# Performance work log

Measured on AMD Instinct MI355X. Metric: run time of the kernel, lower is better.

Reference implementation:

```python
import jax, jax.numpy as jnp
import numpy as np

GROUPS = 8


def setup_inputs() -> dict:
    key = jax.random.key(0)
    k1, k2, k3 = jax.random.split(key, 3)
    B, H, W, Cin, Cout, KH, KW = 32, 56, 56, 256, 256, 3, 3
    inputs = jax.random.normal(k1, (B, H, W, Cin), dtype=jnp.float32)
    # HWIO kernel for grouped conv: input channel dim = Cin // groups
    fan_in = KH * KW * (Cin // GROUPS)
    limit = np.sqrt(6.0 / (fan_in + Cout // GROUPS))  # glorot-ish scale
    kernel = jax.random.uniform(k2, (KH, KW, Cin // GROUPS, Cout), dtype=jnp.float32,
                                minval=-limit, maxval=limit)
    bias = jnp.zeros((Cout,), dtype=jnp.float32)
    return {"inputs": inputs, "kernel": kernel, "bias": bias}


def reference(inputs, kernel, bias):
    # Equivalent to per-group slice + Conv2D + concat: a single grouped conv.
    # inputs: [B,H,W,Cin] NHWC; kernel: [KH,KW,Cin//G,Cout] HWIO
    out = jax.lax.conv_general_dilated(
        inputs, kernel,
        window_strides=(1, 1),
        padding="SAME",
        lhs_dilation=(1, 1),
        rhs_dilation=(1, 1),
        dimension_numbers=("NHWC", "HWIO", "NHWC"),
        feature_group_count=GROUPS,
    )
    out = out + bias  # broadcast over [B,H,W,Cout]
    return out
```

## Files before the change

kernel.cpp:

```cpp
#include <hip/hip_runtime.h>


#define R_ 8
#define TPW 7

typedef __bf16 bf16x8 __attribute__((ext_vector_type(8)));
typedef float floatx4 __attribute__((ext_vector_type(4)));
typedef unsigned short ushortx4 __attribute__((ext_vector_type(4)));

__device__ __forceinline__ unsigned short f2bf(float f) {
    unsigned int u = __builtin_bit_cast(unsigned int, f);
    u += 0x7fffu + ((u >> 16) & 1u);
    return (unsigned short)(u >> 16);
}

__global__ __launch_bounds__(256)
void wprep(const float* __restrict__ wgt, unsigned short* __restrict__ wbf) {
    const int i = blockIdx.x * 256 + threadIdx.x;
    const int co256 = i & 255;
    const int tmp   = i >> 8;
    const int ci    = tmp & 31;
    const int kk    = tmp >> 5;
    const int g  = co256 >> 5;
    const int co = co256 & 31;
    wbf[((g * 9 + kk) * 32 + co) * 32 + ci] = f2bf(wgt[i]);
}

__global__ __launch_bounds__(256, 4)
void gconv_mfma(const float* __restrict__ in, const unsigned short* __restrict__ wbf,
                const float* __restrict__ bias, float* __restrict__ out) {
    const int rt = blockIdx.x;
    const int g  = blockIdx.y;
    const int b  = blockIdx.z;
    const int y0 = rt * R_;

    __shared__ unsigned short lds_in[10 * 58 * 32];

    const int tid = threadIdx.x;

    for (int c = tid; c < 10 * 58 * 8; c += 256) {
        const int row = c / 464;
        const int rem = c - row * 464;
        const int col = rem >> 3;
        const int q   = rem & 7;
        const int gy = y0 - 1 + row;
        const int gx = col - 1;
        float4 v = make_float4(0.f, 0.f, 0.f, 0.f);
        if ((unsigned)gy < 56u && (unsigned)gx < 56u) {
            v = *reinterpret_cast<const float4*>(
                &in[(((b * 56 + gy) * 56 + gx) * 256) + g * 32 + q * 4]);
        }
        ushortx4 p;
        p.x = f2bf(v.x); p.y = f2bf(v.y); p.z = f2bf(v.z); p.w = f2bf(v.w);
        *reinterpret_cast<ushortx4*>(&lds_in[(row * 58 + col) * 32 + q * 4]) = p;
    }

    __syncthreads();

    const int wv   = tid >> 6;
    const int lane = tid & 63;
    const int lc   = lane & 15;
    const int quad = lane >> 4;

    int lane_base[TPW];
#pragma unroll
    for (int t = 0; t < TPW; ++t) {
        const int p  = (wv * TPW + t) * 16 + lc;
        const int yl = p / 56;
        const int xl = p - yl * 56;
        lane_base[t] = (yl * 58 + xl) * 32 + quad * 8;
    }

    const unsigned short* wq = &wbf[((g * 9) * 32) * 32 + quad * 8];

    floatx4 acc[TPW][2];
#pragma unroll
    for (int t = 0; t < TPW; ++t) {
        acc[t][0] = (floatx4)(0.f);
        acc[t][1] = (floatx4)(0.f);
    }

    bf16x8 b0 = *reinterpret_cast<const bf16x8*>(&wq[(0 * 32 + lc) * 32]);
    bf16x8 b1 = *reinterpret_cast<const bf16x8*>(&wq[(0 * 32 + 16 + lc) * 32]);

#pragma unroll
    for (int kk = 0; kk < 9; ++kk) {
        const int ky = kk / 3, kx = kk % 3;
        const int koff = (ky * 58 + kx) * 32;
        bf16x8 nb0 = b0, nb1 = b1;
        if (kk < 8) {
            nb0 = *reinterpret_cast<const bf16x8*>(&wq[((kk + 1) * 32 + lc) * 32]);
            nb1 = *reinterpret_cast<const bf16x8*>(&wq[((kk + 1) * 32 + 16 + lc) * 32]);
        }
#pragma unroll
        for (int t = 0; t < TPW; ++t) {
            const bf16x8 a = *reinterpret_cast<const bf16x8*>(&lds_in[lane_base[t] + koff]);
            acc[t][0] = __builtin_amdgcn_mfma_f32_16x16x32_bf16(a, b0, acc[t][0], 0, 0, 0);
            acc[t][1] = __builtin_amdgcn_mfma_f32_16x16x32_bf16(a, b1, acc[t][1], 0, 0, 0);
        }
        b0 = nb0; b1 = nb1;
    }

    const float bv0 = bias[g * 32 + lc];
    const float bv1 = bias[g * 32 + 16 + lc];
#pragma unroll
    for (int t = 0; t < TPW; ++t) {
#pragma unroll
        for (int r = 0; r < 4; ++r) {
            const int p = (wv * TPW + t) * 16 + quad * 4 + r;
            const int y = p / 56;
            const int x = p - y * 56;
            float* o = &out[(((b * 56) + y0 + y) * 56 + x) * 256 + g * 32];
            o[lc]      = acc[t][0][r] + bv0;
            o[16 + lc] = acc[t][1][r] + bv1;
        }
    }
}

__global__ __launch_bounds__(256, 2)
void gconv_mfma_ldsw(const float* __restrict__ in, const float* __restrict__ wgt,
                     const float* __restrict__ bias, float* __restrict__ out) {
    const int rt = blockIdx.x, g = blockIdx.y, b = blockIdx.z;
    const int y0 = rt * R_;
    __shared__ unsigned short lds_in[10 * 58 * 32];
    __shared__ unsigned short lds_w[9 * 32 * 32];
    const int tid = threadIdx.x;
    for (int i = tid; i < 9 * 32 * 32; i += 256) {
        const int co = i & 31, ci = (i >> 5) & 31, kk = i >> 10;
        lds_w[(kk * 32 + co) * 32 + ci] = f2bf(wgt[(kk * 32 + ci) * 256 + g * 32 + co]);
    }
    for (int c = tid; c < 10 * 58 * 8; c += 256) {
        const int row = c / 464, rem = c - row * 464, col = rem >> 3, q = rem & 7;
        const int gy = y0 - 1 + row, gx = col - 1;
        float4 v = make_float4(0.f, 0.f, 0.f, 0.f);
        if ((unsigned)gy < 56u && (unsigned)gx < 56u)
            v = *reinterpret_cast<const float4*>(&in[(((b * 56 + gy) * 56 + gx) * 256) + g * 32 + q * 4]);
        ushortx4 p;
        p.x = f2bf(v.x); p.y = f2bf(v.y); p.z = f2bf(v.z); p.w = f2bf(v.w);
        *reinterpret_cast<ushortx4*>(&lds_in[(row * 58 + col) * 32 + q * 4]) = p;
    }
    __syncthreads();
    const int wv = tid >> 6, lane = tid & 63, lc = lane & 15, quad = lane >> 4;
    int lane_base[TPW];
#pragma unroll
    for (int t = 0; t < TPW; ++t) {
        const int p = (wv * TPW + t) * 16 + lc;
        const int yl = p / 56, xl = p - yl * 56;
        lane_base[t] = (yl * 58 + xl) * 32 + quad * 8;
    }
    floatx4 acc[TPW][2];
#pragma unroll
    for (int t = 0; t < TPW; ++t) { acc[t][0] = (floatx4)(0.f); acc[t][1] = (floatx4)(0.f); }
#pragma unroll
    for (int kk = 0; kk < 9; ++kk) {
        const int ky = kk / 3, kx = kk % 3;
        const int koff = (ky * 58 + kx) * 32;
        const bf16x8 bf0 = *reinterpret_cast<const bf16x8*>(&lds_w[(kk * 32 + lc) * 32 + quad * 8]);
        const bf16x8 bf1 = *reinterpret_cast<const bf16x8*>(&lds_w[(kk * 32 + 16 + lc) * 32 + quad * 8]);
#pragma unroll
        for (int t = 0; t < TPW; ++t) {
            const bf16x8 a = *reinterpret_cast<const bf16x8*>(&lds_in[lane_base[t] + koff]);
            acc[t][0] = __builtin_amdgcn_mfma_f32_16x16x32_bf16(a, bf0, acc[t][0], 0, 0, 0);
            acc[t][1] = __builtin_amdgcn_mfma_f32_16x16x32_bf16(a, bf1, acc[t][1], 0, 0, 0);
        }
    }
    const float bv0 = bias[g * 32 + lc], bv1 = bias[g * 32 + 16 + lc];
#pragma unroll
    for (int t = 0; t < TPW; ++t)
#pragma unroll
        for (int r = 0; r < 4; ++r) {
            const int p = (wv * TPW + t) * 16 + quad * 4 + r;
            const int y = p / 56, x = p - y * 56;
            float* o = &out[(((b * 56) + y0 + y) * 56 + x) * 256 + g * 32];
            o[lc] = acc[t][0][r] + bv0;
            o[16 + lc] = acc[t][1][r] + bv1;
        }
}

extern "C" void kernel_launch(void* const* d_in, const int* in_sizes, int n_in,
                              void* d_out, int out_size, void* d_ws, size_t ws_size,
                              hipStream_t stream) {
    const float* in   = (const float*)d_in[0];
    const float* wgt  = (const float*)d_in[1];
    const float* bias = (const float*)d_in[2];
    float* out        = (float*)d_out;
    dim3 grid(7, 8, 32);

    if (ws_size >= (size_t)(8 * 9 * 32 * 32 * sizeof(unsigned short))) {
        unsigned short* wbf = (unsigned short*)d_ws;
        wprep<<<dim3(288, 1, 1), dim3(256, 1, 1), 0, stream>>>(wgt, wbf);
        gconv_mfma<<<grid, dim3(256, 1, 1), 0, stream>>>(in, wbf, bias, out);
    } else {
        gconv_mfma_ldsw<<<grid, dim3(256, 1, 1), 0, stream>>>(in, wgt, bias, out);
    }
}
```

Before: 198.1 us.

## Halve row tile, raise occupancy, swap MFMA operands for vectorized float4 stores

The main MFMA kernel now processes 4 output rows per block instead of 8, giving twice as many blocks and a smaller LDS tile. The launch bound is raised to 7 blocks per CU. The 14 pixel tiles are split unevenly across waves (4,4,3,3). MFMA operands are swapped so each lane holds 4 consecutive output channels, which lets the epilogue write float4 stores and read bias as float4 instead of issuing scalar scattered writes. The cost is more halo reloading per output row and idle waves on the shorter tile counts.

```diff
diff --git a/kernel.cpp b/kernel.cpp
--- a/kernel.cpp
+++ b/kernel.cpp
@@ -1,8 +1,8 @@
 #include <hip/hip_runtime.h>
 
 
-#define R_ 8
-#define TPW 7
+#define R_ 4
+#define NCHUNK (6 * 58 * 8)
 
 typedef __bf16 bf16x8 __attribute__((ext_vector_type(8)));
 typedef float floatx4 __attribute__((ext_vector_type(4)));
@@ -26,7 +26,7 @@
     wbf[((g * 9 + kk) * 32 + co) * 32 + ci] = f2bf(wgt[i]);
 }
 
-__global__ __launch_bounds__(256, 4)
+__global__ __launch_bounds__(256, 7)
 void gconv_mfma(const float* __restrict__ in, const unsigned short* __restrict__ wbf,
                 const float* __restrict__ bias, float* __restrict__ out) {
     const int rt = blockIdx.x;
@@ -34,25 +34,29 @@
     const int b  = blockIdx.z;
     const int y0 = rt * R_;
 
-    __shared__ unsigned short lds_in[10 * 58 * 32];
+    __shared__ unsigned short lds_in[6 * 58 * 32];
 
     const int tid = threadIdx.x;
 
-    for (int c = tid; c < 10 * 58 * 8; c += 256) {
-        const int row = c / 464;
-        const int rem = c - row * 464;
-        const int col = rem >> 3;
-        const int q   = rem & 7;
-        const int gy = y0 - 1 + row;
-        const int gx = col - 1;
-        float4 v = make_float4(0.f, 0.f, 0.f, 0.f);
-        if ((unsigned)gy < 56u && (unsigned)gx < 56u) {
-            v = *reinterpret_cast<const float4*>(
-                &in[(((b * 56 + gy) * 56 + gx) * 256) + g * 32 + q * 4]);
-        }
-        ushortx4 p;
-        p.x = f2bf(v.x); p.y = f2bf(v.y); p.z = f2bf(v.z); p.w = f2bf(v.w);
-        *reinterpret_cast<ushortx4*>(&lds_in[(row * 58 + col) * 32 + q * 4]) = p;
+#pragma unroll
+    for (int i = 0; i < 11; ++i) {
+        const int c = tid + (i << 8);
+        if (c < NCHUNK) {
+            const int row = c / 464;
+            const int rem = c - row * 464;
+            const int col = rem >> 3;
+            const int q   = rem & 7;
+            const int gy = y0 - 1 + row;
+            const int gx = col - 1;
+            float4 v = make_float4(0.f, 0.f, 0.f, 0.f);
+            if ((unsigned)gy < 56u && (unsigned)gx < 56u) {
+                v = *reinterpret_cast<const float4*>(
+                    &in[((((b * 56 + gy) * 56 + gx)) << 8) + (g << 5) + (q << 2)]);
+            }
+            ushortx4 p;
+            p.x = f2bf(v.x); p.y = f2bf(v.y); p.z = f2bf(v.z); p.w = f2bf(v.w);
+            *reinterpret_cast<ushortx4*>(&lds_in[(row * 58 + col) * 32 + (q << 2)]) = p;
+        }
     }
 
     __syncthreads();
@@ -62,57 +66,64 @@
     const int lc   = lane & 15;
     const int quad = lane >> 4;
 
-    int lane_base[TPW];
-#pragma unroll
-    for (int t = 0; t < TPW; ++t) {
-        const int p  = (wv * TPW + t) * 16 + lc;
+    const int nt = (wv < 2) ? 4 : 3;
+    const int t0 = (wv < 2) ? (wv * 4) : (8 + (wv - 2) * 3);
+
+    int lane_base[4];
+#pragma unroll
+    for (int t = 0; t < 4; ++t) {
+        const int tt = (t < nt) ? (t0 + t) : 0;
+        const int p  = tt * 16 + lc;
         const int yl = p / 56;
-        const int xl = p - yl * 56;
-        lane_base[t] = (yl * 58 + xl) * 32 + quad * 8;
-    }
-
-    const unsigned short* wq = &wbf[((g * 9) * 32) * 32 + quad * 8];
-
-    floatx4 acc[TPW][2];
-#pragma unroll
-    for (int t = 0; t < TPW; ++t) {
-        acc[t][0] = (floatx4)(0.f);
-        acc[t][1] = (floatx4)(0.f);
-    }
+        lane_base[t] = (yl * 58 + (p - yl * 56)) * 32 + (quad << 3);
+    }
+
+    const unsigned short* wq = &wbf[(g * 9 * 32) * 32 + (quad << 3)];
+
+    floatx4 acc[4][2];
+#pragma unroll
+    for (int t = 0; t < 4; ++t) { acc[t][0] = (floatx4)(0.f); acc[t][1] = (floatx4)(0.f); }
 
     bf16x8 b0 = *reinterpret_cast<const bf16x8*>(&wq[(0 * 32 + lc) * 32]);
     bf16x8 b1 = *reinterpret_cast<const bf16x8*>(&wq[(0 * 32 + 16 + lc) * 32]);
 
 #pragma unroll
     for (int kk = 0; kk < 9; ++kk) {
-        const int ky = kk / 3, kx = kk % 3;
-        const int koff = (ky * 58 + kx) * 32;
+        const int koff = ((kk / 3) * 58 + (kk % 3)) * 32;
         bf16x8 nb0 = b0, nb1 = b1;
         if (kk < 8) {
             nb0 = *reinterpret_cast<const bf16x8*>(&wq[((kk + 1) * 32 + lc) * 32]);
             nb1 = *reinterpret_cast<const bf16x8*>(&wq[((kk + 1) * 32 + 16 + lc) * 32]);
         }
 #pragma unroll
-        for (int t = 0; t < TPW; ++t) {
-            const bf16x8 a = *reinterpret_cast<const bf16x8*>(&lds_in[lane_base[t] + koff]);
-            acc[t][0] = __builtin_amdgcn_mfma_f32_16x16x32_bf16(a, b0, acc[t][0], 0, 0, 0);
-            acc[t][1] = __builtin_amdgcn_mfma_f32_16x16x32_bf16(a, b1, acc[t][1], 0, 0, 0);
+        for (int t = 0; t < 4; ++t) {
+            if (t < nt) {
+                const bf16x8 a = *reinterpret_cast<const bf16x8*>(
+                    &lds_in[lane_base[t] + koff]);
+                acc[t][0] = __builtin_amdgcn_mfma_f32_16x16x32_bf16(b0, a, acc[t][0], 0, 0, 0);
+                acc[t][1] = __builtin_amdgcn_mfma_f32_16x16x32_bf16(b1, a, acc[t][1], 0, 0, 0);
+            }
         }
         b0 = nb0; b1 = nb1;
     }
 
-    const float bv0 = bias[g * 32 + lc];
-    const float bv1 = bias[g * 32 + 16 + lc];
-#pragma unroll
-    for (int t = 0; t < TPW; ++t) {
-#pragma unroll
-        for (int r = 0; r < 4; ++r) {
-            const int p = (wv * TPW + t) * 16 + quad * 4 + r;
+    const float4 bv0 = *reinterpret_cast<const float4*>(&bias[(g << 5) + (quad << 2)]);
+    const float4 bv1 = *reinterpret_cast<const float4*>(&bias[(g << 5) + 16 + (quad << 2)]);
+    const int obase = (((b * 56 + y0) * 56) << 8) + (g << 5) + (quad << 2);
+#pragma unroll
+    for (int t = 0; t < 4; ++t) {
+        if (t < nt) {
+            const int p = (t0 + t) * 16 + lc;
             const int y = p / 56;
             const int x = p - y * 56;
-            float* o = &out[(((b * 56) + y0 + y) * 56 + x) * 256 + g * 32];
-            o[lc]      = acc[t][0][r] + bv0;
-            o[16 + lc] = acc[t][1][r] + bv1;
+            float* o = &out[obase + ((y * 56 + x) << 8)];
+            float4 s0, s1;
+            s0.x = acc[t][0][0] + bv0.x; s0.y = acc[t][0][1] + bv0.y;
+            s0.z = acc[t][0][2] + bv0.z; s0.w = acc[t][0][3] + bv0.w;
+            s1.x = acc[t][1][0] + bv1.x; s1.y = acc[t][1][1] + bv1.y;
+            s1.z = acc[t][1][2] + bv1.z; s1.w = acc[t][1][3] + bv1.w;
+            *reinterpret_cast<float4*>(o)      = s0;
+            *reinterpret_cast<float4*>(o + 16) = s1;
         }
     }
 }
@@ -121,7 +132,7 @@
 void gconv_mfma_ldsw(const float* __restrict__ in, const float* __restrict__ wgt,
                      const float* __restrict__ bias, float* __restrict__ out) {
     const int rt = blockIdx.x, g = blockIdx.y, b = blockIdx.z;
-    const int y0 = rt * R_;
+    const int y0 = rt * 8;
     __shared__ unsigned short lds_in[10 * 58 * 32];
     __shared__ unsigned short lds_w[9 * 32 * 32];
     const int tid = threadIdx.x;
@@ -141,16 +152,16 @@
     }
     __syncthreads();
     const int wv = tid >> 6, lane = tid & 63, lc = lane & 15, quad = lane >> 4;
-    int lane_base[TPW];
-#pragma unroll
-    for (int t = 0; t < TPW; ++t) {
-        const int p = (wv * TPW + t) * 16 + lc;
+    int lane_base[7];
+#pragma unroll
+    for (int t = 0; t < 7; ++t) {
+        const int p = (wv * 7 + t) * 16 + lc;
         const int yl = p / 56, xl = p - yl * 56;
         lane_base[t] = (yl * 58 + xl) * 32 + quad * 8;
     }
-    floatx4 acc[TPW][2];
-#pragma unroll
-    for (int t = 0; t < TPW; ++t) { acc[t][0] = (floatx4)(0.f); acc[t][1] = (floatx4)(0.f); }
+    floatx4 acc[7][2];
+#pragma unroll
+    for (int t = 0; t < 7; ++t) { acc[t][0] = (floatx4)(0.f); acc[t][1] = (floatx4)(0.f); }
 #pragma unroll
     for (int kk = 0; kk < 9; ++kk) {
         const int ky = kk / 3, kx = kk % 3;
@@ -158,7 +169,7 @@
         const bf16x8 bf0 = *reinterpret_cast<const bf16x8*>(&lds_w[(kk * 32 + lc) * 32 + quad * 8]);
         const bf16x8 bf1 = *reinterpret_cast<const bf16x8*>(&lds_w[(kk * 32 + 16 + lc) * 32 + quad * 8]);
 #pragma unroll
-        for (int t = 0; t < TPW; ++t) {
+        for (int t = 0; t < 7; ++t) {
             const bf16x8 a = *reinterpret_cast<const bf16x8*>(&lds_in[lane_base[t] + koff]);
             acc[t][0] = __builtin_amdgcn_mfma_f32_16x16x32_bf16(a, bf0, acc[t][0], 0, 0, 0);
             acc[t][1] = __builtin_amdgcn_mfma_f32_16x16x32_bf16(a, bf1, acc[t][1], 0, 0, 0);
@@ -166,10 +177,10 @@
     }
     const float bv0 = bias[g * 32 + lc], bv1 = bias[g * 32 + 16 + lc];
 #pragma unroll
-    for (int t = 0; t < TPW; ++t)
+    for (int t = 0; t < 7; ++t)
 #pragma unroll
         for (int r = 0; r < 4; ++r) {
-            const int p = (wv * TPW + t) * 16 + quad * 4 + r;
+            const int p = (wv * 7 + t) * 16 + quad * 4 + r;
             const int y = p / 56, x = p - y * 56;
             float* o = &out[(((b * 56) + y0 + y) * 56 + x) * 256 + g * 32];
             o[lc] = acc[t][0][r] + bv0;
@@ -184,13 +195,12 @@
     const float* wgt  = (const float*)d_in[1];
     const float* bias = (const float*)d_in[2];
     float* out        = (float*)d_out;
-    dim3 grid(7, 8, 32);
 
     if (ws_size >= (size_t)(8 * 9 * 32 * 32 * sizeof(unsigned short))) {
         unsigned short* wbf = (unsigned short*)d_ws;
         wprep<<<dim3(288, 1, 1), dim3(256, 1, 1), 0, stream>>>(wgt, wbf);
-        gconv_mfma<<<grid, dim3(256, 1, 1), 0, stream>>>(in, wbf, bias, out);
+        gconv_mfma<<<dim3(14, 8, 32), dim3(256, 1, 1), 0, stream>>>(in, wbf, bias, out);
     } else {
-        gconv_mfma_ldsw<<<grid, dim3(256, 1, 1), 0, stream>>>(in, wgt, bias, out);
-    }
-}
+        gconv_mfma_ldsw<<<dim3(7, 8, 32), dim3(256, 1, 1), 0, stream>>>(in, wgt, bias, out);
+    }
+}
```

After: 204.0 us. +3.0%, slower.
